# Kernel optimization log

Measured on AMD Instinct MI355X. Metric: run time of the kernel, lower is better.

## Reference

```python
import jax, jax.numpy as jnp
import numpy as np

MEAN_X = jnp.array([0.042766, 0.0081577, -0.015818, 9.2993, -0.087913, -3.3231], dtype=jnp.float32).reshape(6, 1)
STD_X = jnp.array([0.4142, 0.3522, 0.2881, 1.474, 0.6553, 0.8728], dtype=jnp.float32).reshape(6, 1)


def conv1d(x, w, b, pad, dil):
    # x: [B,C,L], w: [O,I,K] (torch OIH layout)
    y = jax.lax.conv_general_dilated(
        x, w, window_strides=(1,), padding=[(pad, pad)],
        rhs_dilation=(dil,), dimension_numbers=("NCH", "OIH", "NCH"))
    return y + b[None, :, None]


def setup_inputs() -> dict:
    key = jax.random.key(0)
    ks = jax.random.split(key, 20)
    f32 = jnp.float32
    return {
        "x": jax.random.normal(ks[0], (8192, 7, 200), dtype=f32),
        "calib_mat": 0.05 * jax.random.normal(ks[1], (6, 6), dtype=f32),
        "bias": 0.01 * jax.random.normal(ks[2], (6, 1), dtype=f32),
        "cw1": 0.1 * jax.random.normal(ks[3], (32, 6, 5), dtype=f32),
        "cb1": 0.01 * jax.random.normal(ks[4], (32,), dtype=f32),
        "cw2": 0.1 * jax.random.normal(ks[5], (32, 32, 5), dtype=f32),
        "cb2": 0.01 * jax.random.normal(ks[6], (32,), dtype=f32),
        "cw3": 0.1 * jax.random.normal(ks[7], (32, 32, 5), dtype=f32),
        "cb3": 0.01 * jax.random.normal(ks[8], (32,), dtype=f32),
        "cw4": 0.1 * jax.random.normal(ks[9], (1, 32, 5), dtype=f32),
        "cb4": 0.01 * jax.random.normal(ks[10], (1,), dtype=f32),
        "lw1": 0.05 * jax.random.normal(ks[11], (50, 192), dtype=f32),
        "lb1": 0.01 * jax.random.normal(ks[12], (50,), dtype=f32),
        "lw2": 0.05 * jax.random.normal(ks[13], (50, 50), dtype=f32),
        "lb2": 0.01 * jax.random.normal(ks[14], (50,), dtype=f32),
        "lw3": 0.05 * jax.random.normal(ks[15], (15, 50), dtype=f32),
        "lb3": 0.01 * jax.random.normal(ks[16], (15,), dtype=f32),
    }


def reference(x, calib_mat, bias, cw1, cb1, cw2, cb2, cw3, cb3, cw4, cb4,
              lw1, lb1, lw2, lb2, lw3, lb3):
    gelu = lambda t: jax.nn.gelu(t, approximate=False)  # torch default GELU is erf-based
    B = x.shape[0]
    imu = x[:, 1:, :]                                   # [B,6,L]
    M = jnp.eye(6, dtype=x.dtype) + calib_mat           # [6,6]
    xc = jnp.einsum("ij,bjl->bil", M, imu) + bias       # calibrate
    xn = (xc - MEAN_X) / STD_X                          # normalize
    h = gelu(conv1d(xn, cw1, cb1, pad=4, dil=1))        # [B,32,204]
    h = gelu(conv1d(h, cw2, cb2, pad=4, dil=3))         # [B,32,200]
    h = gelu(conv1d(h, cw3, cb3, pad=4, dil=3))         # [B,32,196]
    h = gelu(conv1d(h, cw4, cb4, pad=4, dil=3))         # [B,1,192]
    f = h.reshape(B, -1)                                # flatten -> [B,192]
    z = gelu(f @ lw1.T + lb1)
    z = gelu(z @ lw2.T + lb2)
    z = (z @ lw3.T + lb3) * 100.0                       # [B,15]
    R = z[:, :9].reshape(B, 3, 3)
    U, _, VT = jnp.linalg.svd(R, full_matrices=False)
    det = jnp.linalg.det(jnp.einsum("bij,bjk->bik", U, VT))  # sign of proper rotation
    scale = jnp.stack([jnp.ones_like(det), jnp.ones_like(det), det], axis=-1)  # diag(1,1,det)
    R_norm = jnp.einsum("bij,bjk->bik", U, VT * scale[:, :, None])
    return jnp.concatenate([R_norm.reshape(B, 9), z[:, 9:]], axis=1)
```

## Files before the change

kernel.cpp:

```cpp
#include <hip/hip_runtime.h>
#include <hip/hip_bf16.h>
#include <math.h>

#define NTHREADS 256
typedef __attribute__((ext_vector_type(8))) short short8;
typedef __attribute__((ext_vector_type(4))) float f32x4;
typedef unsigned short ushort_t;

#define HA    0
#define HB    8480
#define HSTR  40
#define XB    8640
#define XSTR  32
#define SMEM_HW 16960

#define WSF_C1 0
#define WSF_C2 (2*512)
#define WSF_C3 (12*512)
#define WSF_C4 (22*512)
#define WS_F_BYTE_OFF 65536

__device__ __forceinline__ unsigned f2bf(float f) {
    unsigned u = __float_as_uint(f);
    return (u + 0x7FFFu + ((u >> 16) & 1u)) >> 16;
}

__device__ __forceinline__ unsigned pack2bf(float a, float b) {
    __hip_bfloat162 h = __float22bfloat162_rn(make_float2(a, b));
    unsigned u; __builtin_memcpy(&u, &h, 4); return u;
}

__device__ __forceinline__ float gelu_fast(float x) {
    float x2 = x * x;
    float t  = fmaf(0.10294320f, x2, 2.3022082f);
    float e  = __builtin_amdgcn_exp2f(x * t);
    float r  = __builtin_amdgcn_rcpf(e + 1.0f);
    return fmaf(-x, r, x);
}

__device__ __forceinline__ float gelu_exact(float v) {
    return 0.5f * v * (1.0f + erff(v * 0.70710678118654752f));
}

#define JROT(Spp, Sqq, Spq, Sxp, Sxq, Vp0, Vq0, Vp1, Vq1, Vp2, Vq2)          \
    if (fabsf(Spq) > 1e-18f) {                                               \
        float tau = (Sqq - Spp) / (2.0f * Spq);                              \
        float tj = copysignf(1.0f, tau) / (fabsf(tau) + sqrtf(1.0f + tau*tau)); \
        float cj = 1.0f / sqrtf(1.0f + tj*tj);                               \
        float sj = tj * cj;                                                  \
        Spp -= tj * Spq; Sqq += tj * Spq; Spq = 0.0f;                        \
        float tmp0 = Sxp; Sxp = cj*tmp0 - sj*Sxq; Sxq = sj*tmp0 + cj*Sxq;    \
        float tv;                                                            \
        tv = Vp0; Vp0 = cj*tv - sj*Vq0; Vq0 = sj*tv + cj*Vq0;                \
        tv = Vp1; Vp1 = cj*tv - sj*Vq1; Vq1 = sj*tv + cj*Vq1;                \
        tv = Vp2; Vp2 = cj*tv - sj*Vq2; Vq2 = sj*tv + cj*Vq2;                \
    }

__global__ void prep_kernel(const float* __restrict__ cw1,
                            const float* __restrict__ cw2,
                            const float* __restrict__ cw3,
                            const float* __restrict__ cw4,
                            ushort_t* __restrict__ ws)
{
    const int fid = blockIdx.x;
    const int l = threadIdx.x >> 3, j = threadIdx.x & 7;
    const int lo = l & 15, q = l >> 4;
    const int k = q * 8 + j;
    const int pk = ((k >> 2) & 1) * 16 + (k >> 3) * 4 + (k & 3);
    float v = 0.0f;
    if (fid < 2) {
        int m = fid * 16 + lo;
        if (k < 30) { int t = k / 6, c = k - 6 * t; v = cw1[(m * 6 + c) * 5 + t]; }
    } else if (fid < 12) {
        int f = fid - 2, tap = f >> 1, Mt = f & 1, m = Mt * 16 + lo;
        v = cw2[(m * 32 + pk) * 5 + tap];
    } else if (fid < 22) {
        int f = fid - 12, tap = f >> 1, Mt = f & 1, m = Mt * 16 + lo;
        v = cw3[(m * 32 + pk) * 5 + tap];
    } else {
        int tap = fid - 22;
        if (lo == 0) v = cw4[pk * 5 + tap];
    }
    ws[fid * 512 + l * 8 + j] = (ushort_t)f2bf(v);
}

template<bool EDGE>
__device__ __forceinline__ void store_tile(
    ushort_t* __restrict__ dst, const f32x4 a0, const f32x4 a1,
    int n, int Lout, int quad)
{
    ushort_t* row = dst + (4 + n) * HSTR + quad * 8;
    if (EDGE && n >= Lout) {
        *(uint4*)row = make_uint4(0u, 0u, 0u, 0u);
    } else {
        *(uint4*)row = make_uint4(
            pack2bf(gelu_fast(a0[0]), gelu_fast(a0[1])),
            pack2bf(gelu_fast(a0[2]), gelu_fast(a0[3])),
            pack2bf(gelu_fast(a1[0]), gelu_fast(a1[1])),
            pack2bf(gelu_fast(a1[2]), gelu_fast(a1[3])));
    }
}

template<bool TWO, bool EDGEB>
__device__ __forceinline__ void conv_tiles(
    const ushort_t* __restrict__ src, ushort_t* __restrict__ dst,
    const short8 A[5][2], f32x4 b0, f32x4 b1, int Lout,
    int lo16, int quad, int t0)
{
    f32x4 acc00 = b0, acc01 = b1, acc10 = b0, acc11 = b1;
    const int n0a = t0 * 16, n0b = (t0 + 4) * 16;
    const ushort_t* pa = src + (n0a + lo16) * HSTR + quad * 8;
    const ushort_t* pb = src + (n0b + lo16) * HSTR + quad * 8;
    #pragma unroll
    for (int t = 0; t < 5; t++) {
        short8 Ba = *(const short8*)(pa + 3 * HSTR * t);
        acc00 = __builtin_amdgcn_mfma_f32_16x16x32_bf16(A[t][0], Ba, acc00, 0, 0, 0);
        acc01 = __builtin_amdgcn_mfma_f32_16x16x32_bf16(A[t][1], Ba, acc01, 0, 0, 0);
        if (TWO) {
            short8 Bb;
            if (EDGEB) {
                int rb = min(n0b + lo16 + 3 * t, 211);
                Bb = *(const short8*)(src + rb * HSTR + quad * 8);
            } else {
                Bb = *(const short8*)(pb + 3 * HSTR * t);
            }
            acc10 = __builtin_amdgcn_mfma_f32_16x16x32_bf16(A[t][0], Bb, acc10, 0, 0, 0);
            acc11 = __builtin_amdgcn_mfma_f32_16x16x32_bf16(A[t][1], Bb, acc11, 0, 0, 0);
        }
    }
    store_tile<false>(dst, acc00, acc01, n0a + lo16, Lout, quad);
    if (TWO) store_tile<EDGEB>(dst, acc10, acc11, n0b + lo16, Lout, quad);
}

template<int LAYER>
__device__ __forceinline__ void conv_mfma(
    const ushort_t* __restrict__ src, ushort_t* __restrict__ dst,
    const ushort_t* __restrict__ wsf, const float* __restrict__ bias,
    int Lout, int lane, int wave)
{
    const int lo16 = lane & 15, quad = lane >> 4;
    short8 A[5][2];
    #pragma unroll
    for (int t = 0; t < 5; t++) {
        A[t][0] = *(const short8*)(wsf + (t * 2 + 0) * 512 + lane * 8);
        A[t][1] = *(const short8*)(wsf + (t * 2 + 1) * 512 + lane * 8);
    }
    f32x4 b0, b1;
    #pragma unroll
    for (int r = 0; r < 4; r++) { b0[r] = bias[quad * 4 + r]; b1[r] = bias[16 + quad * 4 + r]; }
    conv_tiles<true, false>(src, dst, A, b0, b1, Lout, lo16, quad, wave);
    if (wave == 0) conv_tiles<true, true>(src, dst, A, b0, b1, Lout, lo16, quad, 8);
    else           conv_tiles<false, false>(src, dst, A, b0, b1, Lout, lo16, quad, wave + 8);
}

__device__ __forceinline__ void conv1_packed(
    const ushort_t* __restrict__ xb, ushort_t* __restrict__ dst,
    const ushort_t* __restrict__ wsf, const float* __restrict__ bias,
    int lane, int wave)
{
    const int lo16 = lane & 15, quad = lane >> 4;
    const short8 A0 = *(const short8*)(wsf + 0 * 512 + lane * 8);
    const short8 A1 = *(const short8*)(wsf + 1 * 512 + lane * 8);
    f32x4 b0, b1;
    #pragma unroll
    for (int r = 0; r < 4; r++) { b0[r] = bias[quad * 4 + r]; b1[r] = bias[16 + quad * 4 + r]; }
    f32x4 a0[3], a1[3];
    #pragma unroll
    for (int u = 0; u < 3; u++) {
        const int n = (wave + 4 * u) * 16 + lo16;
        short8 B = *(const short8*)(xb + n * XSTR + quad * 8);
        a0[u] = __builtin_amdgcn_mfma_f32_16x16x32_bf16(A0, B, b0, 0, 0, 0);
        a1[u] = __builtin_amdgcn_mfma_f32_16x16x32_bf16(A1, B, b1, 0, 0, 0);
    }
    #pragma unroll
    for (int u = 0; u < 3; u++)
        store_tile<false>(dst, a0[u], a1[u], (wave + 4 * u) * 16 + lo16, 204, quad);
    if (wave == 0) {
        const int n = 192 + lo16;
        short8 B = *(const short8*)(xb + n * XSTR + quad * 8);
        f32x4 e0 = __builtin_amdgcn_mfma_f32_16x16x32_bf16(A0, B, b0, 0, 0, 0);
        f32x4 e1 = __builtin_amdgcn_mfma_f32_16x16x32_bf16(A1, B, b1, 0, 0, 0);
        store_tile<true>(dst, e0, e1, n, 204, quad);
    }
}

__global__ void __launch_bounds__(NTHREADS, 4)
rminet_conv_kernel(const float* __restrict__ x,
                   const float* __restrict__ calib,
                   const float* __restrict__ biasv,
                   const float* __restrict__ cb1, const float* __restrict__ cb2,
                   const float* __restrict__ cb3, const float* __restrict__ cb4,
                   const ushort_t* __restrict__ wsp,
                   float* __restrict__ F)
{
    __shared__ __align__(16) ushort_t smh[SMEM_HW];
    const int tid  = threadIdx.x;
    const int b    = blockIdx.x;
    const int lane = tid & 63;
    const int wave = __builtin_amdgcn_readfirstlane(tid >> 6);

    {
        uint4* p = (uint4*)smh;
        for (int i = tid; i < 988; i += NTHREADS) {
            int idx = (i < 20) ? i
                    : (i < 80) ? 1000 + (i - 20)
                    : (i < 948) ? 1060 + (i - 80)
                    : 2080 + (i - 948);
            p[idx] = make_uint4(0u, 0u, 0u, 0u);
        }
    }
    __syncthreads();

    if (tid < 200) {
        const float* xc = x + (size_t)b * 1400 + 200 + tid;
        float v[6];
        #pragma unroll
        for (int ch = 0; ch < 6; ch++) v[ch] = xc[ch * 200];
        const float MEANS[6]  = {0.042766f, 0.0081577f, -0.015818f, 9.2993f, -0.087913f, -3.3231f};
        const float INVSTD[6] = {1.f/0.4142f, 1.f/0.3522f, 1.f/0.2881f, 1.f/1.474f, 1.f/0.6553f, 1.f/0.8728f};
        float xn[6];
        #pragma unroll
        for (int i = 0; i < 6; i++) {
            float acc = biasv[i];
            #pragma unroll
            for (int jj = 0; jj < 6; jj++) {
                float m = calib[i * 6 + jj] + ((i == jj) ? 1.0f : 0.0f);
                acc = fmaf(m, v[jj], acc);
            }
            xn[i] = (acc - MEANS[i]) * INVSTD[i];
        }
        const unsigned d0 = pack2bf(xn[0], xn[1]);
        const unsigned d1 = pack2bf(xn[2], xn[3]);
        const unsigned d2 = pack2bf(xn[4], xn[5]);
        const int trot = tid & 3;
        #pragma unroll
        for (int tt = 0; tt < 5; tt++) {
            int t = tt + trot; if (t >= 5) t -= 5;
            ushort_t* qp = smh + XB + (tid + 4 - t) * XSTR + t * 6;
            *(unsigned*)(qp + 0) = d0;
            *(unsigned*)(qp + 2) = d1;
            *(unsigned*)(qp + 4) = d2;
        }
    }
    __syncthreads();

    conv1_packed(smh + XB, smh + HA, wsp + WSF_C1, cb1, lane, wave);
    __syncthreads();
    conv_mfma<2>(smh + HA, smh + HB, wsp + WSF_C2, cb2, 200, lane, wave);
    __syncthreads();
    conv_mfma<3>(smh + HB, smh + HA, wsp + WSF_C3, cb3, 196, lane, wave);
    if (tid < 20) ((uint4*)smh)[1000 + tid] = make_uint4(0u, 0u, 0u, 0u);
    __syncthreads();

    {
        const int lo16 = lane & 15, quad = lane >> 4;
        short8 A4[5];
        #pragma unroll
        for (int t = 0; t < 5; t++)
            A4[t] = *(const short8*)(wsp + WSF_C4 + t * 512 + lane * 8);
        f32x4 acc[3];
        #pragma unroll
        for (int u = 0; u < 3; u++) acc[u] = (f32x4){0.f, 0.f, 0.f, 0.f};
        const ushort_t* p4[3];
        #pragma unroll
        for (int u = 0; u < 3; u++)
            p4[u] = smh + HA + ((wave + 4 * u) * 16 + lo16) * HSTR + quad * 8;
        #pragma unroll
        for (int t = 0; t < 5; t++) {
            #pragma unroll
            for (int u = 0; u < 3; u++) {
                short8 B = *(const short8*)(p4[u] + 3 * HSTR * t);
                acc[u] = __builtin_amdgcn_mfma_f32_16x16x32_bf16(A4[t], B, acc[u], 0, 0, 0);
            }
        }
        if (quad == 0) {
            const float c4 = cb4[0];
            #pragma unroll
            for (int u = 0; u < 3; u++) {
                int n = (wave + 4 * u) * 16 + lo16;
                F[(size_t)b * 192 + n] = gelu_fast(acc[u][0] + c4);
            }
        }
    }
}

#define TLW1 0
#define TLW2 2400
#define TLW3 3050
#define TFQ  3245
#define TZ1F 16052
#define TZVF 16884
#define TSM_FLOATS 17156

__global__ void __launch_bounds__(256)
rminet_tail_kernel(const float* __restrict__ F,
                   const float* __restrict__ lw1, const float* __restrict__ lb1,
                   const float* __restrict__ lw2, const float* __restrict__ lb2,
                   const float* __restrict__ lw3, const float* __restrict__ lb3,
                   float* __restrict__ out)
{
    __shared__ __align__(16) float smf[TSM_FLOATS];
    float4* smq = (float4*)smf;
    const int tid  = threadIdx.x;
    const int lane = tid & 63;
    const int g    = __builtin_amdgcn_readfirstlane(tid >> 6);
    const int i0   = blockIdx.x * 16;
    const int ib   = g * 4;

    for (int idx = tid; idx < 2400; idx += 256) {
        int j4 = idx / 50, c = idx - j4 * 50;
        smq[TLW1 + idx] = *(const float4*)&lw1[c * 192 + 4 * j4];
    }
    for (int idx = tid; idx < 650; idx += 256) {
        int j4 = idx / 50, c = idx - j4 * 50;
        const float* wr = lw2 + c * 50 + 4 * j4;
        float4 w;
        w.x = wr[0]; w.y = wr[1];
        w.z = (4 * j4 + 2 < 50) ? wr[2] : 0.0f;
        w.w = (4 * j4 + 3 < 50) ? wr[3] : 0.0f;
        smq[TLW2 + idx] = w;
    }
    for (int idx = tid; idx < 195; idx += 256) {
        int j4 = idx / 15, c = idx - j4 * 15;
        const float* wr = lw3 + c * 50 + 4 * j4;
        float4 w;
        w.x = wr[0]; w.y = wr[1];
        w.z = (4 * j4 + 2 < 50) ? wr[2] : 0.0f;
        w.w = (4 * j4 + 3 < 50) ? wr[3] : 0.0f;
        smq[TLW3 + idx] = w;
    }
    {
        const float4* G4 = (const float4*)F + (size_t)i0 * 48;
        for (int idx = tid; idx < 768; idx += 256) smq[TFQ + idx] = G4[idx];
    }
    if (tid < 32) smf[TZ1F + (tid >> 1) * 52 + 50 + (tid & 1)] = 0.0f;
    __syncthreads();

    const int cc = min(lane, 49);

    {
        float a0, a1, a2, a3;
        a0 = a1 = a2 = a3 = lb1[cc];
        for (int j4 = 0; j4 < 48; j4++) {
            float4 w = smq[TLW1 + j4 * 50 + cc];
            float4 f0 = smq[TFQ + (ib + 0) * 48 + j4];
            float4 f1 = smq[TFQ + (ib + 1) * 48 + j4];
            float4 f2 = smq[TFQ + (ib + 2) * 48 + j4];
            float4 f3 = smq[TFQ + (ib + 3) * 48 + j4];
            a0 = fmaf(w.x, f0.x, fmaf(w.y, f0.y, fmaf(w.z, f0.z, fmaf(w.w, f0.w, a0))));
            a1 = fmaf(w.x, f1.x, fmaf(w.y, f1.y, fmaf(w.z, f1.z, fmaf(w.w, f1.w, a1))));
            a2 = fmaf(w.x, f2.x, fmaf(w.y, f2.y, fmaf(w.z, f2.z, fmaf(w.w, f2.w, a2))));
            a3 = fmaf(w.x, f3.x, fmaf(w.y, f3.y, fmaf(w.z, f3.z, fmaf(w.w, f3.w, a3))));
        }
        if (lane < 50) {
            smf[TZ1F + (ib + 0) * 52 + lane] = gelu_exact(a0);
            smf[TZ1F + (ib + 1) * 52 + lane] = gelu_exact(a1);
            smf[TZ1F + (ib + 2) * 52 + lane] = gelu_exact(a2);
            smf[TZ1F + (ib + 3) * 52 + lane] = gelu_exact(a3);
        }
    }

    {
        float a0, a1, a2, a3;
        a0 = a1 = a2 = a3 = lb2[cc];
        for (int j4 = 0; j4 < 13; j4++) {
            float4 w = smq[TLW2 + j4 * 50 + cc];
            float4 z0 = *(const float4*)&smf[TZ1F + (ib + 0) * 52 + 4 * j4];
            float4 z1 = *(const float4*)&smf[TZ1F + (ib + 1) * 52 + 4 * j4];
            float4 z2 = *(const float4*)&smf[TZ1F + (ib + 2) * 52 + 4 * j4];
            float4 z3 = *(const float4*)&smf[TZ1F + (ib + 3) * 52 + 4 * j4];
            a0 = fmaf(w.x, z0.x, fmaf(w.y, z0.y, fmaf(w.z, z0.z, fmaf(w.w, z0.w, a0))));
            a1 = fmaf(w.x, z1.x, fmaf(w.y, z1.y, fmaf(w.z, z1.z, fmaf(w.w, z1.w, a1))));
            a2 = fmaf(w.x, z2.x, fmaf(w.y, z2.y, fmaf(w.z, z2.z, fmaf(w.w, z2.w, a2))));
            a3 = fmaf(w.x, z3.x, fmaf(w.y, z3.y, fmaf(w.z, z3.z, fmaf(w.w, z3.w, a3))));
        }
        if (lane < 50) {
            smf[TZ1F + (ib + 0) * 52 + lane] = gelu_exact(a0);
            smf[TZ1F + (ib + 1) * 52 + lane] = gelu_exact(a1);
            smf[TZ1F + (ib + 2) * 52 + lane] = gelu_exact(a2);
            smf[TZ1F + (ib + 3) * 52 + lane] = gelu_exact(a3);
        }
    }

    {
        const int c3 = min(lane, 14);
        float a0, a1, a2, a3;
        a0 = a1 = a2 = a3 = lb3[c3];
        for (int j4 = 0; j4 < 13; j4++) {
            float4 w = smq[TLW3 + j4 * 15 + c3];
            float4 z0 = *(const float4*)&smf[TZ1F + (ib + 0) * 52 + 4 * j4];
            float4 z1 = *(const float4*)&smf[TZ1F + (ib + 1) * 52 + 4 * j4];
            float4 z2 = *(const float4*)&smf[TZ1F + (ib + 2) * 52 + 4 * j4];
            float4 z3 = *(const float4*)&smf[TZ1F + (ib + 3) * 52 + 4 * j4];
            a0 = fmaf(w.x, z0.x, fmaf(w.y, z0.y, fmaf(w.z, z0.z, fmaf(w.w, z0.w, a0))));
            a1 = fmaf(w.x, z1.x, fmaf(w.y, z1.y, fmaf(w.z, z1.z, fmaf(w.w, z1.w, a1))));
            a2 = fmaf(w.x, z2.x, fmaf(w.y, z2.y, fmaf(w.z, z2.z, fmaf(w.w, z2.w, a2))));
            a3 = fmaf(w.x, z3.x, fmaf(w.y, z3.y, fmaf(w.z, z3.z, fmaf(w.w, z3.w, a3))));
        }
        if (lane < 15) {
            smf[TZVF + (ib + 0) * 17 + lane] = a0 * 100.0f;
            smf[TZVF + (ib + 1) * 17 + lane] = a1 * 100.0f;
            smf[TZVF + (ib + 2) * 17 + lane] = a2 * 100.0f;
            smf[TZVF + (ib + 3) * 17 + lane] = a3 * 100.0f;
        }
    }
    __syncthreads();

    if (g == 0 && lane < 16) {
        const float* zv = &smf[TZVF + lane * 17];
        float* ob = out + (size_t)(i0 + lane) * 15;
        #pragma unroll
        for (int c = 9; c < 15; c++) ob[c] = zv[c];

        const float A00 = zv[0], A01 = zv[1], A02 = zv[2];
        const float A10 = zv[3], A11 = zv[4], A12 = zv[5];
        const float A20 = zv[6], A21 = zv[7], A22 = zv[8];
        float S00 = A00*A00 + A10*A10 + A20*A20;
        float S01 = A00*A01 + A10*A11 + A20*A21;
        float S02 = A00*A02 + A10*A12 + A20*A22;
        float S11 = A01*A01 + A11*A11 + A21*A21;
        float S12 = A01*A02 + A11*A12 + A21*A22;
        float S22 = A02*A02 + A12*A12 + A22*A22;
        float V00=1.f, V01=0.f, V02=0.f;
        float V10=0.f, V11=1.f, V12=0.f;
        float V20=0.f, V21=0.f, V22=1.f;
        #pragma unroll
        for (int sweep = 0; sweep < 8; sweep++) {
            JROT(S00, S11, S01, S02, S12, V00, V01, V10, V11, V20, V21)
            JROT(S00, S22, S02, S01, S12, V00, V02, V10, V12, V20, V22)
            JROT(S11, S22, S12, S01, S02, V01, V02, V11, V12, V21, V22)
        }
        float e0 = S00, e1 = S11, e2 = S22;
        float va0=V00, va1=V10, va2=V20;
        float vb0=V01, vb1=V11, vb2=V21;
        float vc0=V02, vc1=V12, vc2=V22;
        float sgn = 1.0f, tq;
        if (e0 < e1) { tq=e0;e0=e1;e1=tq; tq=va0;va0=vb0;vb0=tq; tq=va1;va1=vb1;vb1=tq; tq=va2;va2=vb2;vb2=tq; sgn=-sgn; }
        if (e1 < e2) { tq=e1;e1=e2;e2=tq; tq=vb0;vb0=vc0;vc0=tq; tq=vb1;vb1=vc1;vc1=tq; tq=vb2;vb2=vc2;vc2=tq; sgn=-sgn; }
        if (e0 < e1) { tq=e0;e0=e1;e1=tq; tq=va0;va0=vb0;vb0=tq; tq=va1;va1=vb1;vb1=tq; tq=va2;va2=vb2;vb2=tq; sgn=-sgn; }
        vc0 *= sgn; vc1 *= sgn; vc2 *= sgn;
        float u10 = A00*va0 + A01*va1 + A02*va2;
        float u11 = A10*va0 + A11*va1 + A12*va2;
        float u12 = A20*va0 + A21*va1 + A22*va2;
        float n1 = sqrtf(u10*u10 + u11*u11 + u12*u12);
        float rn1 = (n1 > 1e-20f) ? 1.0f / n1 : 0.0f;
        u10 *= rn1; u11 *= rn1; u12 *= rn1;
        float u20 = A00*vb0 + A01*vb1 + A02*vb2;
        float u21 = A10*vb0 + A11*vb1 + A12*vb2;
        float u22 = A20*vb0 + A21*vb1 + A22*vb2;
        float d12 = u20*u10 + u21*u11 + u22*u12;
        u20 -= d12*u10; u21 -= d12*u11; u22 -= d12*u12;
        float n2 = sqrtf(u20*u20 + u21*u21 + u22*u22);
        float rn2 = (n2 > 1e-20f) ? 1.0f / n2 : 0.0f;
        u20 *= rn2; u21 *= rn2; u22 *= rn2;
        float u30 = u11*u22 - u12*u21;
        float u31 = u12*u20 - u10*u22;
        float u32 = u10*u21 - u11*u20;
        ob[0] = u10*va0 + u20*vb0 + u30*vc0;
        ob[1] = u10*va1 + u20*vb1 + u30*vc1;
        ob[2] = u10*va2 + u20*vb2 + u30*vc2;
        ob[3] = u11*va0 + u21*vb0 + u31*vc0;
        ob[4] = u11*va1 + u21*vb1 + u31*vc1;
        ob[5] = u11*va2 + u21*vb2 + u31*vc2;
        ob[6] = u12*va0 + u22*vb0 + u32*vc0;
        ob[7] = u12*va1 + u22*vb1 + u32*vc1;
        ob[8] = u12*va2 + u22*vb2 + u32*vc2;
    }
}

extern "C" void kernel_launch(void* const* d_in, const int* in_sizes, int n_in,
                              void* d_out, int out_size, void* d_ws, size_t ws_size,
                              hipStream_t stream) {
    (void)n_in; (void)out_size; (void)ws_size;
    const float* x     = (const float*)d_in[0];
    const float* calib = (const float*)d_in[1];
    const float* biasv = (const float*)d_in[2];
    const float* cw1   = (const float*)d_in[3];
    const float* cb1   = (const float*)d_in[4];
    const float* cw2   = (const float*)d_in[5];
    const float* cb2   = (const float*)d_in[6];
    const float* cw3   = (const float*)d_in[7];
    const float* cb3   = (const float*)d_in[8];
    const float* cw4   = (const float*)d_in[9];
    const float* cb4   = (const float*)d_in[10];
    const float* lw1   = (const float*)d_in[11];
    const float* lb1   = (const float*)d_in[12];
    const float* lw2   = (const float*)d_in[13];
    const float* lb2   = (const float*)d_in[14];
    const float* lw3   = (const float*)d_in[15];
    const float* lb3   = (const float*)d_in[16];
    float* out = (float*)d_out;
    ushort_t* wsh = (ushort_t*)d_ws;
    float* Fb = (float*)((char*)d_ws + WS_F_BYTE_OFF);
    const int B = in_sizes[0] / 1400;

    hipLaunchKernelGGL(prep_kernel, dim3(27), dim3(512), 0, stream,
                       cw1, cw2, cw3, cw4, wsh);
    hipLaunchKernelGGL(rminet_conv_kernel, dim3(B), dim3(NTHREADS), 0, stream,
                       x, calib, biasv, cb1, cb2, cb3, cb4,
                       (const ushort_t*)wsh, Fb);
    hipLaunchKernelGGL(rminet_tail_kernel, dim3(B / 16), dim3(256), 0, stream,
                       (const float*)Fb, lw1, lb1, lw2, lb2, lw3, lb3, out);
}
```

Before: 206.4 us.

## Pre-pack MLP weights in prep kernel and read lw1/features from global

The prep kernel gains extra blocks that repack lw1/lw2/lw3 into the float4-transposed layout once per call, writing them to workspace. The tail kernel now stages only lw2/lw3 in LDS and reads lw1 and the conv features directly from global (cache), shrinking shared memory from ~68KB to ~18KB so more blocks can be resident (launch bounds hint 6). This trades LDS staging and its barrier for per-iteration global/L2 loads in the first layer.

```diff
diff --git a/kernel.cpp b/kernel.cpp
--- a/kernel.cpp
+++ b/kernel.cpp
@@ -60,9 +60,38 @@
                             const float* __restrict__ cw2,
                             const float* __restrict__ cw3,
                             const float* __restrict__ cw4,
-                            ushort_t* __restrict__ ws)
+                            const float* __restrict__ lw1,
+                            const float* __restrict__ lw2,
+                            const float* __restrict__ lw3,
+                            ushort_t* __restrict__ ws,
+                            float4* __restrict__ twb)
 {
     const int fid = blockIdx.x;
+    if (fid >= 27) {
+        const int idx = (fid - 27) * 512 + threadIdx.x;
+        if (idx < 2400) {
+            int j4 = idx / 50, c = idx - 50 * j4;
+            const float* p = lw1 + c * 192 + 4 * j4;
+            twb[idx] = make_float4(p[0], p[1], p[2], p[3]);
+        } else if (idx < 3050) {
+            int r = idx - 2400, j4 = r / 50, c = r - 50 * j4;
+            const float* p = lw2 + c * 50 + 4 * j4;
+            float4 w;
+            w.x = p[0]; w.y = p[1];
+            w.z = (4 * j4 + 2 < 50) ? p[2] : 0.0f;
+            w.w = (4 * j4 + 3 < 50) ? p[3] : 0.0f;
+            twb[idx] = w;
+        } else if (idx < 3245) {
+            int r = idx - 3050, j4 = r / 15, c = r - 15 * j4;
+            const float* p = lw3 + c * 50 + 4 * j4;
+            float4 w;
+            w.x = p[0]; w.y = p[1];
+            w.z = (4 * j4 + 2 < 50) ? p[2] : 0.0f;
+            w.w = (4 * j4 + 3 < 50) ? p[3] : 0.0f;
+            twb[idx] = w;
+        }
+        return;
+    }
     const int l = threadIdx.x >> 3, j = threadIdx.x & 7;
     const int lo = l & 15, q = l >> 4;
     const int k = q * 8 + j;
@@ -284,19 +313,18 @@
     }
 }
 
-#define TLW1 0
-#define TLW2 2400
-#define TLW3 3050
-#define TFQ  3245
-#define TZ1F 16052
-#define TZVF 16884
-#define TSM_FLOATS 17156
-
-__global__ void __launch_bounds__(256)
+#define TLW2q 0
+#define TLW3q 650
+#define TZ1F  3380
+#define TZVF  4212
+#define TSM_FLOATS 4484
+
+__global__ void __launch_bounds__(256, 6)
 rminet_tail_kernel(const float* __restrict__ F,
-                   const float* __restrict__ lw1, const float* __restrict__ lb1,
-                   const float* __restrict__ lw2, const float* __restrict__ lb2,
-                   const float* __restrict__ lw3, const float* __restrict__ lb3,
+                   const float4* __restrict__ twb,
+                   const float* __restrict__ lb1,
+                   const float* __restrict__ lb2,
+                   const float* __restrict__ lb3,
                    float* __restrict__ out)
 {
     __shared__ __align__(16) float smf[TSM_FLOATS];
@@ -307,46 +335,23 @@
     const int i0   = blockIdx.x * 16;
     const int ib   = g * 4;
 
-    for (int idx = tid; idx < 2400; idx += 256) {
-        int j4 = idx / 50, c = idx - j4 * 50;
-        smq[TLW1 + idx] = *(const float4*)&lw1[c * 192 + 4 * j4];
-    }
-    for (int idx = tid; idx < 650; idx += 256) {
-        int j4 = idx / 50, c = idx - j4 * 50;
-        const float* wr = lw2 + c * 50 + 4 * j4;
-        float4 w;
-        w.x = wr[0]; w.y = wr[1];
-        w.z = (4 * j4 + 2 < 50) ? wr[2] : 0.0f;
-        w.w = (4 * j4 + 3 < 50) ? wr[3] : 0.0f;
-        smq[TLW2 + idx] = w;
-    }
-    for (int idx = tid; idx < 195; idx += 256) {
-        int j4 = idx / 15, c = idx - j4 * 15;
-        const float* wr = lw3 + c * 50 + 4 * j4;
-        float4 w;
-        w.x = wr[0]; w.y = wr[1];
-        w.z = (4 * j4 + 2 < 50) ? wr[2] : 0.0f;
-        w.w = (4 * j4 + 3 < 50) ? wr[3] : 0.0f;
-        smq[TLW3 + idx] = w;
-    }
+    for (int idx = tid; idx < 845; idx += 256) smq[idx] = twb[2400 + idx];
+    if (tid < 32) smf[TZ1F + (tid >> 1) * 52 + 50 + (tid & 1)] = 0.0f;
+    __syncthreads();
+
+    const int cc = min(lane, 49);
+    const float4* Fq = (const float4*)F;
+
     {
-        const float4* G4 = (const float4*)F + (size_t)i0 * 48;
-        for (int idx = tid; idx < 768; idx += 256) smq[TFQ + idx] = G4[idx];
-    }
-    if (tid < 32) smf[TZ1F + (tid >> 1) * 52 + 50 + (tid & 1)] = 0.0f;
-    __syncthreads();
-
-    const int cc = min(lane, 49);
-
-    {
+        const float4* lw1q = twb;
         float a0, a1, a2, a3;
         a0 = a1 = a2 = a3 = lb1[cc];
         for (int j4 = 0; j4 < 48; j4++) {
-            float4 w = smq[TLW1 + j4 * 50 + cc];
-            float4 f0 = smq[TFQ + (ib + 0) * 48 + j4];
-            float4 f1 = smq[TFQ + (ib + 1) * 48 + j4];
-            float4 f2 = smq[TFQ + (ib + 2) * 48 + j4];
-            float4 f3 = smq[TFQ + (ib + 3) * 48 + j4];
+            float4 w = lw1q[j4 * 50 + cc];
+            float4 f0 = Fq[(size_t)(i0 + ib + 0) * 48 + j4];
+            float4 f1 = Fq[(size_t)(i0 + ib + 1) * 48 + j4];
+            float4 f2 = Fq[(size_t)(i0 + ib + 2) * 48 + j4];
+            float4 f3 = Fq[(size_t)(i0 + ib + 3) * 48 + j4];
             a0 = fmaf(w.x, f0.x, fmaf(w.y, f0.y, fmaf(w.z, f0.z, fmaf(w.w, f0.w, a0))));
             a1 = fmaf(w.x, f1.x, fmaf(w.y, f1.y, fmaf(w.z, f1.z, fmaf(w.w, f1.w, a1))));
             a2 = fmaf(w.x, f2.x, fmaf(w.y, f2.y, fmaf(w.z, f2.z, fmaf(w.w, f2.w, a2))));
@@ -364,7 +369,7 @@
         float a0, a1, a2, a3;
         a0 = a1 = a2 = a3 = lb2[cc];
         for (int j4 = 0; j4 < 13; j4++) {
-            float4 w = smq[TLW2 + j4 * 50 + cc];
+            float4 w = smq[TLW2q + j4 * 50 + cc];
             float4 z0 = *(const float4*)&smf[TZ1F + (ib + 0) * 52 + 4 * j4];
             float4 z1 = *(const float4*)&smf[TZ1F + (ib + 1) * 52 + 4 * j4];
             float4 z2 = *(const float4*)&smf[TZ1F + (ib + 2) * 52 + 4 * j4];
@@ -387,7 +392,7 @@
         float a0, a1, a2, a3;
         a0 = a1 = a2 = a3 = lb3[c3];
         for (int j4 = 0; j4 < 13; j4++) {
-            float4 w = smq[TLW3 + j4 * 15 + c3];
+            float4 w = smq[TLW3q + j4 * 15 + c3];
             float4 z0 = *(const float4*)&smf[TZ1F + (ib + 0) * 52 + 4 * j4];
             float4 z1 = *(const float4*)&smf[TZ1F + (ib + 1) * 52 + 4 * j4];
             float4 z2 = *(const float4*)&smf[TZ1F + (ib + 2) * 52 + 4 * j4];
@@ -491,14 +496,15 @@
     const float* lb3   = (const float*)d_in[16];
     float* out = (float*)d_out;
     ushort_t* wsh = (ushort_t*)d_ws;
+    const int B = in_sizes[0] / 1400;
     float* Fb = (float*)((char*)d_ws + WS_F_BYTE_OFF);
-    const int B = in_sizes[0] / 1400;
-
-    hipLaunchKernelGGL(prep_kernel, dim3(27), dim3(512), 0, stream,
-                       cw1, cw2, cw3, cw4, wsh);
+    float4* twb = (float4*)((char*)d_ws + WS_F_BYTE_OFF + (size_t)B * 768);
+
+    hipLaunchKernelGGL(prep_kernel, dim3(34), dim3(512), 0, stream,
+                       cw1, cw2, cw3, cw4, lw1, lw2, lw3, wsh, twb);
     hipLaunchKernelGGL(rminet_conv_kernel, dim3(B), dim3(NTHREADS), 0, stream,
                        x, calib, biasv, cb1, cb2, cb3, cb4,
                        (const ushort_t*)wsh, Fb);
     hipLaunchKernelGGL(rminet_tail_kernel, dim3(B / 16), dim3(256), 0, stream,
-                       (const float*)Fb, lw1, lb1, lw2, lb2, lw3, lb3, out);
-}
+                       (const float*)Fb, (const float4*)twb, lb1, lb2, lb3, out);
+}
```

Result: slower. 233.5 us (+13.2%).
